# Optimization experiments

Hardware: AMD Instinct MI355X
Metric: run time of the kernel (lower is better)

## Reference

```python
import jax, jax.numpy as jnp
import numpy as np

N_NODES = 100000
E_RAW = 1600000
SKIP_COEFF = 0.5
NEG_SLOPE = 0.2
BN_EPS = 1e-5


def _gat_conv(x, src, dst, W, a_src, a_dst, b, heads, out_ch):
    # PyG GATConv (concat=True). x: [N, F_in], W: [F_in, heads*out_ch]
    N = x.shape[0]
    h = (x @ W).reshape(N, heads, out_ch)                      # [N,H,C]
    alpha_src = jnp.sum(h * a_src, axis=-1)                    # [N,H]
    alpha_dst = jnp.sum(h * a_dst, axis=-1)                    # [N,H]
    e = jax.nn.leaky_relu(alpha_src[src] + alpha_dst[dst], NEG_SLOPE)  # [E,H]
    # segment softmax over incoming edges of each destination node
    m = jax.ops.segment_max(e, dst, num_segments=N)            # [N,H]
    p = jnp.exp(e - m[dst])
    denom = jax.ops.segment_sum(p, dst, num_segments=N)        # [N,H]
    alpha = p / denom[dst]                                      # [E,H]
    out = jax.ops.segment_sum(h[src] * alpha[:, :, None], dst, num_segments=N)
    return out.reshape(N, heads * out_ch) + b


def _bn(x, gamma, beta):
    # BatchNorm1d, training-mode batch statistics (biased variance)
    mu = jnp.mean(x, axis=0)
    var = jnp.var(x, axis=0)
    return (x - mu) * jax.lax.rsqrt(var + BN_EPS) * gamma + beta


def _glorot(key, shape):
    fan = shape[0] + shape[-1] if len(shape) == 2 else shape[-1] * 2
    s = jnp.sqrt(6.0 / fan)
    return jax.random.uniform(key, shape, jnp.float32, -s, s)


def setup_inputs() -> dict:
    key = jax.random.key(0)
    ks = jax.random.split(key, 24)
    x = jax.random.normal(ks[0], (N_NODES, 128), jnp.float32)
    edge_index = jax.random.randint(ks[1], (2, E_RAW), 0, N_NODES, jnp.int64)
    d = {"x": x, "edge_index": edge_index}
    # conv0: 128 -> (4 heads x 32); conv1,conv2: 128 -> (4x32); conv3: 128 -> (1x64)
    dims = [(128, 4, 32), (128, 4, 32), (128, 4, 32), (128, 1, 64)]
    ki = 2
    for l, (fin, H, C) in enumerate(dims):
        d[f"W{l}"] = _glorot(ks[ki], (fin, H * C)); ki += 1
        d[f"as{l}"] = _glorot(ks[ki], (H, C)); ki += 1
        d[f"ad{l}"] = _glorot(ks[ki], (H, C)); ki += 1
        d[f"b{l}"] = jnp.zeros((H * C,), jnp.float32)
    d["g1"] = jnp.ones((128,), jnp.float32)
    d["be1"] = jnp.zeros((128,), jnp.float32)
    d["g2"] = jnp.ones((128,), jnp.float32)
    d["be2"] = jnp.zeros((128,), jnp.float32)
    return d


def reference(x, edge_index, W0, as0, ad0, b0, W1, as1, ad1, b1,
              W2, as2, ad2, b2, W3, as3, ad3, b3, g1, be1, g2, be2):
    N = x.shape[0]
    loops = jnp.arange(N, dtype=edge_index.dtype)
    src = jnp.concatenate([edge_index[0], loops])  # add self-loops (PyG default)
    dst = jnp.concatenate([edge_index[1], loops])

    h = _gat_conv(x, src, dst, W0, as0, ad0, b0, 4, 32)        # [N,128]
    h_skip = h
    # i = 1
    h = _gat_conv(h, src, dst, W1, as1, ad1, b1, 4, 32)
    h = jax.nn.relu(_bn(h, g1, be1))
    out1 = h
    # i = 2 (skip branch)
    h = _gat_conv(h, src, dst, W2, as2, ad2, b2, 4, 32)
    h = _bn(h, g2, be2) + SKIP_COEFF * h_skip
    h = jax.nn.relu(h)
    out2 = h

    h = out1 + out2
    return _gat_conv(h, src, dst, W3, as3, ad3, b3, 1, 64)      # [N,64]
```

## Files before the change

### kernel.cpp

```cpp
#include <hip/hip_runtime.h>
#include <cstdint>
#include <cstddef>


typedef unsigned int uint;
typedef unsigned short ushort_t;
typedef __attribute__((ext_vector_type(8))) short bf16x8_t;
typedef __attribute__((ext_vector_type(4))) float f32x4_t;

__device__ __forceinline__ float leaky(float e) { return e < 0.f ? 0.2f * e : e; }
__device__ __forceinline__ float bflo(uint u) { return __uint_as_float(u << 16); }
__device__ __forceinline__ float bfhi(uint u) { return __uint_as_float(u & 0xffff0000u); }
__device__ __forceinline__ ushort_t f2bf(float f) {
  uint u = __float_as_uint(f);
  u += 0x7fffu + ((u >> 16) & 1u);
  return (ushort_t)(u >> 16);
}
__device__ __forceinline__ float bf2f(ushort_t h) { return __uint_as_float((uint)h << 16); }
__device__ __forceinline__ uint pack2(float a, float b) {
  return (uint)f2bf(a) | ((uint)f2bf(b) << 16);
}


__global__ __launch_bounds__(256) void k_deg(const int* __restrict__ ei, int ER, int ET,
                                             int* __restrict__ deg) {
  int e = blockIdx.x * 256 + threadIdx.x;
  if (e >= ET) return;
  int d = (e < ER) ? ei[ER + e] : (e - ER);
  atomicAdd(&deg[d], 1);
}

__global__ __launch_bounds__(256) void k_scan1(const int* __restrict__ deg, int* __restrict__ rp,
                                               int* __restrict__ bsums, int n) {
  __shared__ int sh[256];
  int tid = threadIdx.x;
  int base = blockIdx.x * 2048 + tid * 8;
  int pre[8];
  int s = 0;
#pragma unroll
  for (int j = 0; j < 8; ++j) {
    int idx = base + j;
    int v = (idx < n) ? deg[idx] : 0;
    pre[j] = s;
    s += v;
  }
  sh[tid] = s;
  __syncthreads();
  for (int d = 1; d < 256; d <<= 1) {
    int t = (tid >= d) ? sh[tid - d] : 0;
    __syncthreads();
    if (tid >= d) sh[tid] += t;
    __syncthreads();
  }
  int excl = sh[tid] - s;
#pragma unroll
  for (int j = 0; j < 8; ++j) {
    int idx = base + j;
    if (idx < n) rp[idx] = excl + pre[j];
  }
  if (tid == 255) bsums[blockIdx.x] = sh[255];
}

__global__ void k_scan2(int* bsums, int nb) {
  for (int i = 1; i < nb; ++i) bsums[i] += bsums[i - 1];
}

__global__ __launch_bounds__(256) void k_scan3(int* __restrict__ rp, const int* __restrict__ bsums,
                                               int n, int ET) {
  int i = blockIdx.x * 256 + threadIdx.x;
  if (i > n) return;
  if (i == n) { rp[n] = ET; return; }
  int b = i >> 11;
  if (b > 0) rp[i] += bsums[b - 1];
}

__global__ __launch_bounds__(256) void k_scatter(const int* __restrict__ ei, int ER, int ET,
                                                 const int* __restrict__ rp, int* __restrict__ fill,
                                                 int* __restrict__ col) {
  int e = blockIdx.x * 256 + threadIdx.x;
  if (e >= ET) return;
  int s, d;
  if (e < ER) { s = ei[e]; d = ei[ER + e]; } else { s = e - ER; d = s; }
  int pos = rp[d] + atomicAdd(&fill[d], 1);
  col[pos] = s;
}


__global__ __launch_bounds__(256) void k_prepW(const float* __restrict__ W0,
                                               const float* __restrict__ W1,
                                               const float* __restrict__ W2,
                                               const float* __restrict__ W3,
                                               ushort_t* __restrict__ Wthi,
                                               ushort_t* __restrict__ Wtlo) {
  int id = blockIdx.x * 256 + threadIdx.x;
  int l = id >> 14;
  if (l >= 4) return;
  int t = id & 16383;
  int j = t >> 7, k = t & 127;
  const float* W = (l == 0) ? W0 : (l == 1) ? W1 : (l == 2) ? W2 : W3;
  int cols = (l == 3) ? 64 : 128;
  if (j >= cols) return;
  float v = W[(size_t)k * cols + j];
  ushort_t hi = f2bf(v);
  float rem = v - bf2f(hi);
  Wthi[(size_t)l * 16384 + j * 128 + k] = hi;
  Wtlo[(size_t)l * 16384 + j * 128 + k] = f2bf(rem);
}


__global__ __launch_bounds__(256) void k_split(const float* __restrict__ in,
                                               uint* __restrict__ hi2, uint* __restrict__ lo2,
                                               int n4) {
  int i = blockIdx.x * 256 + threadIdx.x;
  if (i >= n4) return;
  float4 v = ((const float4*)in)[i];
  ushort_t hx = f2bf(v.x), hy = f2bf(v.y), hz = f2bf(v.z), hw = f2bf(v.w);
  uint2 h = make_uint2((uint)hx | ((uint)hy << 16), (uint)hz | ((uint)hw << 16));
  uint2 l = make_uint2(pack2(v.x - bf2f(hx), v.y - bf2f(hy)),
                       pack2(v.z - bf2f(hz), v.w - bf2f(hw)));
  ((uint2*)hi2)[i] = h;
  ((uint2*)lo2)[i] = l;
}


template <int COLS, int H>
__global__ __launch_bounds__(256) void k_mm(const ushort_t* __restrict__ Ahi,
                                            const ushort_t* __restrict__ Alo,
                                            const ushort_t* __restrict__ Wthi,
                                            const ushort_t* __restrict__ Wtlo,
                                            const float* __restrict__ aS,
                                            const float* __restrict__ aD,
                                            ushort_t* __restrict__ hbf,
                                            float* __restrict__ asg,
                                            float* __restrict__ adg, int N) {
  constexpr int NB = COLS / 16;
  __shared__ __align__(16) ushort_t sWhi[COLS * 136];
  __shared__ __align__(16) ushort_t sWlo[COLS * 136];
  int tid = threadIdx.x;
  int lane = tid & 63, wv = tid >> 6;
  int lj = lane & 15, lg = lane >> 4;
  int r0 = blockIdx.x * 64 + wv * 16;

  for (int idx = tid; idx < COLS * 16; idx += 256) {
    int j = idx >> 4, seg = idx & 15;
    uint4 vh = *(const uint4*)(Wthi + (size_t)j * 128 + seg * 8);
    uint4 vl = *(const uint4*)(Wtlo + (size_t)j * 128 + seg * 8);
    *(uint4*)&sWhi[j * 136 + seg * 8] = vh;
    *(uint4*)&sWlo[j * 136 + seg * 8] = vl;
  }
  __syncthreads();

  f32x4_t acc[NB];
#pragma unroll
  for (int cb = 0; cb < NB; ++cb) acc[cb] = (f32x4_t){0.f, 0.f, 0.f, 0.f};

  int rowc = r0 + lj; if (rowc >= N) rowc = N - 1;
  const ushort_t* apH = Ahi + (size_t)rowc * 128 + lg * 8;
  const ushort_t* apL = Alo + (size_t)rowc * 128 + lg * 8;

#pragma unroll
  for (int kc = 0; kc < 4; ++kc) {
    bf16x8_t ah = *(const bf16x8_t*)(apH + kc * 32);
    bf16x8_t al = *(const bf16x8_t*)(apL + kc * 32);
#pragma unroll
    for (int cb = 0; cb < NB; ++cb) {
      int boff = (cb * 16 + lj) * 136 + kc * 32 + lg * 8;
      bf16x8_t bh = *(const bf16x8_t*)&sWhi[boff];
      bf16x8_t bl = *(const bf16x8_t*)&sWlo[boff];
      acc[cb] = __builtin_amdgcn_mfma_f32_16x16x32_bf16(ah, bh, acc[cb], 0, 0, 0);
      acc[cb] = __builtin_amdgcn_mfma_f32_16x16x32_bf16(al, bh, acc[cb], 0, 0, 0);
      acc[cb] = __builtin_amdgcn_mfma_f32_16x16x32_bf16(ah, bl, acc[cb], 0, 0, 0);
    }
  }

  float asv[NB], adv[NB];
#pragma unroll
  for (int cb = 0; cb < NB; ++cb) {
    asv[cb] = aS[cb * 16 + lj];
    adv[cb] = aD[cb * 16 + lj];
  }
#pragma unroll
  for (int reg = 0; reg < 4; ++reg) {
    int row = r0 + lg * 4 + reg;
    if (H == 4) {
      float ps[4] = {0.f, 0.f, 0.f, 0.f}, pd[4] = {0.f, 0.f, 0.f, 0.f};
#pragma unroll
      for (int cb = 0; cb < NB; ++cb) {
        int h = cb >> 1;
        ps[h] += acc[cb][reg] * asv[cb];
        pd[h] += acc[cb][reg] * adv[cb];
      }
#pragma unroll
      for (int m = 1; m < 16; m <<= 1) {
#pragma unroll
        for (int h = 0; h < 4; ++h) {
          ps[h] += __shfl_xor(ps[h], m);
          pd[h] += __shfl_xor(pd[h], m);
        }
      }
      if (lj == 0 && row < N) {
        *(float4*)(asg + (size_t)row * 4) = make_float4(ps[0], ps[1], ps[2], ps[3]);
        *(float4*)(adg + (size_t)row * 4) = make_float4(pd[0], pd[1], pd[2], pd[3]);
      }
    } else {
      float ps = 0.f, pd = 0.f;
#pragma unroll
      for (int cb = 0; cb < NB; ++cb) {
        ps += acc[cb][reg] * asv[cb];
        pd += acc[cb][reg] * adv[cb];
      }
#pragma unroll
      for (int m = 1; m < 16; m <<= 1) {
        ps += __shfl_xor(ps, m);
        pd += __shfl_xor(pd, m);
      }
      if (lj == 0 && row < N) { asg[row] = ps; adg[row] = pd; }
    }
  }

  __syncthreads();
  ushort_t* bnc = sWhi + wv * (16 * 136);
#pragma unroll
  for (int cb = 0; cb < NB; ++cb)
#pragma unroll
    for (int reg = 0; reg < 4; ++reg)
      bnc[(lg * 4 + reg) * 136 + cb * 16 + lj] = f2bf(acc[cb][reg]);
  constexpr int UPR = COLS / 8;
  constexpr int NPASS = 16 * UPR / 64;
#pragma unroll
  for (int p = 0; p < NPASS; ++p) {
    int u = p * 64 + lane;
    int rl = u / UPR, sg = u % UPR;
    if (r0 + rl < N)
      *(uint4*)(hbf + (size_t)(r0 + rl) * COLS + sg * 8) = *(const uint4*)&bnc[rl * 136 + sg * 8];
  }
}


template <int H, int C, int MODE>
__global__ __launch_bounds__(256) void k_agg(const int* __restrict__ rp, const int* __restrict__ col,
                                             const ushort_t* __restrict__ hbf,
                                             const float* __restrict__ asg,
                                             const float* __restrict__ adg,
                                             const float* __restrict__ bias,
                                             float* __restrict__ out,
                                             uint* __restrict__ outp,
                                             uint* __restrict__ ohi, uint* __restrict__ olo,
                                             int N) {
  constexpr int HC = H * C;
  constexpr int LPE = HC / 8;
  constexpr int EPI = 64 / LPE;
  __shared__ float shp[4][64 * H];
  int lane = threadIdx.x & 63;
  int wv = threadIdx.x >> 6;
  int n = blockIdx.x * 4 + wv;
  if (n >= N) return;

  int sub = lane / LPE;
  int le = lane % LPE;
  int ch0 = le * 8;
  int head = (H == 4) ? (ch0 >> 5) : 0;

  float d0 = 0.f, d1 = 0.f, d2 = 0.f, d3 = 0.f;
  if (H == 4) {
    float4 t = *(const float4*)(adg + (size_t)n * 4);
    d0 = t.x; d1 = t.y; d2 = t.z; d3 = t.w;
  } else {
    d0 = adg[n];
  }

  int s0 = rp[n], s1 = rp[n + 1];
  float denom = 0.f;
  float a[8];
#pragma unroll
  for (int k = 0; k < 8; ++k) a[k] = 0.f;

  for (int base = s0; base < s1; base += 64) {
    int lim = s1 - base; if (lim > 64) lim = 64;
    int j = base + lane;
    bool valid = j < s1;
    int cj = valid ? col[j] : 0;

    if (H == 4) {
      float4 t = *(const float4*)(asg + (size_t)cj * 4);
      float4 p;
      p.x = valid ? __expf(leaky(t.x + d0)) : 0.f;
      p.y = valid ? __expf(leaky(t.y + d1)) : 0.f;
      p.z = valid ? __expf(leaky(t.z + d2)) : 0.f;
      p.w = valid ? __expf(leaky(t.w + d3)) : 0.f;
      *(float4*)&shp[wv][lane * 4] = p;
    } else {
      float t = asg[cj];
      shp[wv][lane] = valid ? __expf(leaky(t + d0)) : 0.f;
    }
    __builtin_amdgcn_sched_barrier(0);

    for (int i = 0; i < lim; i += EPI) {
      int e = i + sub;
      int s = __shfl(cj, e);
      float p = (H == 4) ? shp[wv][e * 4 + head] : shp[wv][e];
      uint4 hv = *(const uint4*)(hbf + (size_t)s * HC + ch0);
      a[0] += p * bflo(hv.x); a[1] += p * bfhi(hv.x);
      a[2] += p * bflo(hv.y); a[3] += p * bfhi(hv.y);
      a[4] += p * bflo(hv.z); a[5] += p * bfhi(hv.z);
      a[6] += p * bflo(hv.w); a[7] += p * bfhi(hv.w);
      denom += p;
    }
  }

#pragma unroll
  for (int m = LPE; m < 64; m <<= 1) {
#pragma unroll
    for (int k = 0; k < 8; ++k) a[k] += __shfl_xor(a[k], m);
    denom += __shfl_xor(denom, m);
  }

  if (sub != 0) return;
  float inv = 1.f / denom;
  float o[8];
#pragma unroll
  for (int k = 0; k < 8; ++k) o[k] = a[k] * inv + bias[ch0 + k];

  if (MODE == 0) {
    float4 w0 = make_float4(o[0], o[1], o[2], o[3]);
    float4 w1 = make_float4(o[4], o[5], o[6], o[7]);
    *(float4*)(out + (size_t)n * HC + ch0) = w0;
    *(float4*)(out + (size_t)n * HC + ch0 + 4) = w1;
  } else {
    uint hw[4], lw[4];
#pragma unroll
    for (int k = 0; k < 4; ++k) {
      ushort_t hx = f2bf(o[2 * k]), hy = f2bf(o[2 * k + 1]);
      hw[k] = (uint)hx | ((uint)hy << 16);
      lw[k] = pack2(o[2 * k] - bf2f(hx), o[2 * k + 1] - bf2f(hy));
    }
    uint4 hv = make_uint4(hw[0], hw[1], hw[2], hw[3]);
    uint4 lv = make_uint4(lw[0], lw[1], lw[2], lw[3]);
    *(uint4*)(outp + (size_t)n * 64 + le * 4) = hv;
    *(uint4*)(ohi + (size_t)n * 64 + le * 4) = hv;
    *(uint4*)(olo + (size_t)n * 64 + le * 4) = lv;
  }
}


__global__ __launch_bounds__(512) void k_bnstats1(const float* __restrict__ t,
                                                  float* __restrict__ p1, float* __restrict__ p2,
                                                  int N) {
  __shared__ float ls[4][128], ls2[4][128];
  int c = threadIdx.x & 127, q = threadIdx.x >> 7;
  float s = 0.f, s2 = 0.f;
  for (int r = blockIdx.x * 4 + q; r < N; r += gridDim.x * 4) {
    float v = t[(size_t)r * 128 + c];
    s += v;
    s2 += v * v;
  }
  ls[q][c] = s; ls2[q][c] = s2;
  __syncthreads();
  if (q == 0) {
    s = ls[0][c] + ls[1][c] + ls[2][c] + ls[3][c];
    s2 = ls2[0][c] + ls2[1][c] + ls2[2][c] + ls2[3][c];
    p1[blockIdx.x * 128 + c] = s;
    p2[blockIdx.x * 128 + c] = s2;
  }
}

__global__ void k_bnstats2(const float* __restrict__ p1, const float* __restrict__ p2,
                           float* __restrict__ mu, float* __restrict__ rstd, int G, int N) {
  int c = threadIdx.x;
  float s = 0.f, s2 = 0.f;
  for (int b = 0; b < G; ++b) { s += p1[b * 128 + c]; s2 += p2[b * 128 + c]; }
  float m = s / (float)N;
  float var = s2 / (float)N - m * m;
  mu[c] = m;
  rstd[c] = rsqrtf(var + 1e-5f);
}

__global__ __launch_bounds__(256) void k_bnapply1(const float* __restrict__ t,
                                                  const float* __restrict__ mu,
                                                  const float* __restrict__ rstd,
                                                  const float* __restrict__ g,
                                                  const float* __restrict__ be,
                                                  uint* __restrict__ o1p,
                                                  uint* __restrict__ ohi, uint* __restrict__ olo,
                                                  int n4) {
  int i = blockIdx.x * 256 + threadIdx.x;
  if (i >= n4) return;
  float4 v = ((const float4*)t)[i];
  int c = (i & 31) * 4;
  float4 r;
  r.x = fmaxf((v.x - mu[c + 0]) * rstd[c + 0] * g[c + 0] + be[c + 0], 0.f);
  r.y = fmaxf((v.y - mu[c + 1]) * rstd[c + 1] * g[c + 1] + be[c + 1], 0.f);
  r.z = fmaxf((v.z - mu[c + 2]) * rstd[c + 2] * g[c + 2] + be[c + 2], 0.f);
  r.w = fmaxf((v.w - mu[c + 3]) * rstd[c + 3] * g[c + 3] + be[c + 3], 0.f);
  ushort_t hx = f2bf(r.x), hy = f2bf(r.y), hz = f2bf(r.z), hw = f2bf(r.w);
  uint2 h = make_uint2((uint)hx | ((uint)hy << 16), (uint)hz | ((uint)hw << 16));
  ((uint2*)o1p)[i] = h;
  ((uint2*)ohi)[i] = h;
  ((uint2*)olo)[i] = make_uint2(pack2(r.x - bf2f(hx), r.y - bf2f(hy)),
                                pack2(r.z - bf2f(hz), r.w - bf2f(hw)));
}

__global__ __launch_bounds__(256) void k_bnapply2(const float* __restrict__ t,
                                                  const uint* __restrict__ skp,
                                                  const uint* __restrict__ o1p,
                                                  const float* __restrict__ mu,
                                                  const float* __restrict__ rstd,
                                                  const float* __restrict__ g,
                                                  const float* __restrict__ be,
                                                  uint* __restrict__ ohi, uint* __restrict__ olo,
                                                  int n4) {
  int i = blockIdx.x * 256 + threadIdx.x;
  if (i >= n4) return;
  float4 v = ((const float4*)t)[i];
  uint2 sku = ((const uint2*)skp)[i];
  uint2 o1u = ((const uint2*)o1p)[i];
  int c = (i & 31) * 4;
  float4 r;
  r.x = bflo(o1u.x) + fmaxf((v.x - mu[c + 0]) * rstd[c + 0] * g[c + 0] + be[c + 0] + 0.5f * bflo(sku.x), 0.f);
  r.y = bfhi(o1u.x) + fmaxf((v.y - mu[c + 1]) * rstd[c + 1] * g[c + 1] + be[c + 1] + 0.5f * bfhi(sku.x), 0.f);
  r.z = bflo(o1u.y) + fmaxf((v.z - mu[c + 2]) * rstd[c + 2] * g[c + 2] + be[c + 2] + 0.5f * bflo(sku.y), 0.f);
  r.w = bfhi(o1u.y) + fmaxf((v.w - mu[c + 3]) * rstd[c + 3] * g[c + 3] + be[c + 3] + 0.5f * bfhi(sku.y), 0.f);
  ushort_t hx = f2bf(r.x), hy = f2bf(r.y), hz = f2bf(r.z), hw = f2bf(r.w);
  ((uint2*)ohi)[i] = make_uint2((uint)hx | ((uint)hy << 16), (uint)hz | ((uint)hw << 16));
  ((uint2*)olo)[i] = make_uint2(pack2(r.x - bf2f(hx), r.y - bf2f(hy)),
                                pack2(r.z - bf2f(hz), r.w - bf2f(hw)));
}


extern "C" void kernel_launch(void* const* d_in, const int* in_sizes, int n_in,
                              void* d_out, int out_size, void* d_ws, size_t ws_size,
                              hipStream_t stream) {
  const float* x = (const float*)d_in[0];
  const int* ei = (const int*)d_in[1];
  const float* W[4]  = {(const float*)d_in[2], (const float*)d_in[6],
                        (const float*)d_in[10], (const float*)d_in[14]};
  const float* AS[4] = {(const float*)d_in[3], (const float*)d_in[7],
                        (const float*)d_in[11], (const float*)d_in[15]};
  const float* AD[4] = {(const float*)d_in[4], (const float*)d_in[8],
                        (const float*)d_in[12], (const float*)d_in[16]};
  const float* B[4]  = {(const float*)d_in[5], (const float*)d_in[9],
                        (const float*)d_in[13], (const float*)d_in[17]};
  const float* g1 = (const float*)d_in[18];
  const float* be1 = (const float*)d_in[19];
  const float* g2 = (const float*)d_in[20];
  const float* be2 = (const float*)d_in[21];

  const int N = in_sizes[0] / 128;
  const int ER = in_sizes[1] / 2;
  const int ET = ER + N;

  char* ws = (char*)d_ws;
  size_t off = 0;
  auto carve = [&](size_t bytes) {
    size_t o = off;
    off = (off + bytes + 255) & ~(size_t)255;
    return (void*)(ws + o);
  };
  int* rowptr     = (int*)carve((size_t)(N + 1) * 4);
  int* col        = (int*)carve((size_t)ET * 4);
  int* bsums      = (int*)carve(64 * 4);
  float* asg      = (float*)carve((size_t)N * 4 * 4);
  float* adg      = (float*)carve((size_t)N * 4 * 4);
  ushort_t* hbf   = (ushort_t*)carve((size_t)N * 128 * 2);
  ushort_t* ahi   = (ushort_t*)carve((size_t)N * 128 * 2);
  ushort_t* alo   = (ushort_t*)carve((size_t)N * 128 * 2);
  uint* skipb     = (uint*)carve((size_t)N * 64 * 4);
  uint* out1b     = (uint*)carve((size_t)N * 64 * 4);
  float* tbuf     = (float*)carve((size_t)N * 128 * 4);
  ushort_t* Wthi  = (ushort_t*)carve(4 * 16384 * 2);
  ushort_t* Wtlo  = (ushort_t*)carve(4 * 16384 * 2);
  float* p1       = (float*)carve(128 * 128 * 4);
  float* p2       = (float*)carve(128 * 128 * 4);
  float* mu       = (float*)carve(128 * 4);
  float* rstd     = (float*)carve(128 * 4);
  int* fill       = (int*)asg;
  (void)ws_size;

  const int nb = (N + 2047) / 2048;
  const int gE = (ET + 255) / 256;
  const int gN4 = (N + 3) / 4;
  const int gM = (N + 63) / 64;
  const int n4 = N * 32;
  const int gP = (n4 + 255) / 256;

  hipMemsetAsync(fill, 0, (size_t)N * 4, stream);
  k_deg<<<gE, 256, 0, stream>>>(ei, ER, ET, fill);
  k_scan1<<<nb, 256, 0, stream>>>(fill, rowptr, bsums, N);
  k_scan2<<<1, 1, 0, stream>>>(bsums, nb);
  k_scan3<<<(N + 256) / 256, 256, 0, stream>>>(rowptr, bsums, N, ET);
  hipMemsetAsync(fill, 0, (size_t)N * 4, stream);
  k_scatter<<<gE, 256, 0, stream>>>(ei, ER, ET, rowptr, fill, col);
  k_prepW<<<256, 256, 0, stream>>>(W[0], W[1], W[2], W[3], Wthi, Wtlo);
  k_split<<<gP, 256, 0, stream>>>(x, (uint*)ahi, (uint*)alo, n4);

  k_mm<128, 4><<<gM, 256, 0, stream>>>(ahi, alo, Wthi, Wtlo, AS[0], AD[0], hbf, asg, adg, N);
  k_agg<4, 32, 1><<<gN4, 256, 0, stream>>>(rowptr, col, hbf, asg, adg, B[0], nullptr,
                                           skipb, (uint*)ahi, (uint*)alo, N);

  k_mm<128, 4><<<gM, 256, 0, stream>>>(ahi, alo, Wthi + 16384, Wtlo + 16384, AS[1], AD[1],
                                       hbf, asg, adg, N);
  k_agg<4, 32, 0><<<gN4, 256, 0, stream>>>(rowptr, col, hbf, asg, adg, B[1], tbuf,
                                           nullptr, nullptr, nullptr, N);
  k_bnstats1<<<128, 512, 0, stream>>>(tbuf, p1, p2, N);
  k_bnstats2<<<1, 128, 0, stream>>>(p1, p2, mu, rstd, 128, N);
  k_bnapply1<<<gP, 256, 0, stream>>>(tbuf, mu, rstd, g1, be1, out1b, (uint*)ahi, (uint*)alo, n4);

  k_mm<128, 4><<<gM, 256, 0, stream>>>(ahi, alo, Wthi + 2 * 16384, Wtlo + 2 * 16384, AS[2], AD[2],
                                       hbf, asg, adg, N);
  k_agg<4, 32, 0><<<gN4, 256, 0, stream>>>(rowptr, col, hbf, asg, adg, B[2], tbuf,
                                           nullptr, nullptr, nullptr, N);
  k_bnstats1<<<128, 512, 0, stream>>>(tbuf, p1, p2, N);
  k_bnstats2<<<1, 128, 0, stream>>>(p1, p2, mu, rstd, 128, N);
  k_bnapply2<<<gP, 256, 0, stream>>>(tbuf, skipb, out1b, mu, rstd, g2, be2,
                                     (uint*)ahi, (uint*)alo, n4);

  k_mm<64, 1><<<gM, 256, 0, stream>>>(ahi, alo, Wthi + 3 * 16384, Wtlo + 3 * 16384, AS[3], AD[3],
                                      hbf, asg, adg, N);
  k_agg<1, 64, 0><<<gN4, 256, 0, stream>>>(rowptr, col, hbf, asg, adg, B[3], (float*)d_out,
                                           nullptr, nullptr, nullptr, N);
}
```

Baseline: 916.2 us.

## Fold attention vectors into weight matrix and fuse input split into GEMM

Precomputes W·a_src and W·a_dst as extra columns appended to each transposed weight matrix, so the attention logits come straight out of the MFMA accumulators. This replaces the per-row dot products and shuffle reductions. The first layer now converts fp32 x to bf16 hi/lo pairs inside the GEMM, which removes the separate split kernel and its round trip through memory. BN statistics use 256 blocks instead of 128, and the changed algebra order slightly alters the rounding of the logits.

```diff
diff --git a/kernel.cpp b/kernel.cpp
--- a/kernel.cpp
+++ b/kernel.cpp
@@ -90,58 +90,63 @@
                                                const float* __restrict__ W1,
                                                const float* __restrict__ W2,
                                                const float* __restrict__ W3,
+                                               const float* __restrict__ AS0,
+                                               const float* __restrict__ AS1,
+                                               const float* __restrict__ AS2,
+                                               const float* __restrict__ AS3,
+                                               const float* __restrict__ AD0,
+                                               const float* __restrict__ AD1,
+                                               const float* __restrict__ AD2,
+                                               const float* __restrict__ AD3,
                                                ushort_t* __restrict__ Wthi,
                                                ushort_t* __restrict__ Wtlo) {
   int id = blockIdx.x * 256 + threadIdx.x;
-  int l = id >> 14;
-  if (l >= 4) return;
-  int t = id & 16383;
+  if (id >= 4 * 144 * 128) return;
+  int l = id / (144 * 128);
+  int t = id % (144 * 128);
   int j = t >> 7, k = t & 127;
-  const float* W = (l == 0) ? W0 : (l == 1) ? W1 : (l == 2) ? W2 : W3;
+  const float* W  = (l == 0) ? W0  : (l == 1) ? W1  : (l == 2) ? W2  : W3;
+  const float* aS = (l == 0) ? AS0 : (l == 1) ? AS1 : (l == 2) ? AS2 : AS3;
+  const float* aD = (l == 0) ? AD0 : (l == 1) ? AD1 : (l == 2) ? AD2 : AD3;
   int cols = (l == 3) ? 64 : 128;
-  if (j >= cols) return;
-  float v = W[(size_t)k * cols + j];
+  int H = (l == 3) ? 1 : 4;
+  int C = (l == 3) ? 64 : 32;
+  float v = 0.f;
+  if (j < cols) {
+    v = W[(size_t)k * cols + j];
+  } else if (j < cols + H) {
+    int h = j - cols;
+    for (int c = 0; c < C; ++c) v += W[(size_t)k * cols + h * C + c] * aS[h * C + c];
+  } else if (j < cols + 2 * H) {
+    int h = j - cols - H;
+    for (int c = 0; c < C; ++c) v += W[(size_t)k * cols + h * C + c] * aD[h * C + c];
+  }
   ushort_t hi = f2bf(v);
   float rem = v - bf2f(hi);
-  Wthi[(size_t)l * 16384 + j * 128 + k] = hi;
-  Wtlo[(size_t)l * 16384 + j * 128 + k] = f2bf(rem);
-}
-
-
-__global__ __launch_bounds__(256) void k_split(const float* __restrict__ in,
-                                               uint* __restrict__ hi2, uint* __restrict__ lo2,
-                                               int n4) {
-  int i = blockIdx.x * 256 + threadIdx.x;
-  if (i >= n4) return;
-  float4 v = ((const float4*)in)[i];
-  ushort_t hx = f2bf(v.x), hy = f2bf(v.y), hz = f2bf(v.z), hw = f2bf(v.w);
-  uint2 h = make_uint2((uint)hx | ((uint)hy << 16), (uint)hz | ((uint)hw << 16));
-  uint2 l = make_uint2(pack2(v.x - bf2f(hx), v.y - bf2f(hy)),
-                       pack2(v.z - bf2f(hz), v.w - bf2f(hw)));
-  ((uint2*)hi2)[i] = h;
-  ((uint2*)lo2)[i] = l;
-}
-
-
-template <int COLS, int H>
-__global__ __launch_bounds__(256) void k_mm(const ushort_t* __restrict__ Ahi,
+  Wthi[(size_t)l * 144 * 128 + j * 128 + k] = hi;
+  Wtlo[(size_t)l * 144 * 128 + j * 128 + k] = f2bf(rem);
+}
+
+
+template <int COLS, int CP, int H, int SRC>
+__global__ __launch_bounds__(256) void k_mm(const float* __restrict__ Xf,
+                                            const ushort_t* __restrict__ Ahi,
                                             const ushort_t* __restrict__ Alo,
                                             const ushort_t* __restrict__ Wthi,
                                             const ushort_t* __restrict__ Wtlo,
-                                            const float* __restrict__ aS,
-                                            const float* __restrict__ aD,
                                             ushort_t* __restrict__ hbf,
                                             float* __restrict__ asg,
                                             float* __restrict__ adg, int N) {
-  constexpr int NB = COLS / 16;
-  __shared__ __align__(16) ushort_t sWhi[COLS * 136];
-  __shared__ __align__(16) ushort_t sWlo[COLS * 136];
+  constexpr int NB = CP / 16;
+  constexpr int NBH = COLS / 16;
+  __shared__ __align__(16) ushort_t sWhi[CP * 136];
+  __shared__ __align__(16) ushort_t sWlo[CP * 136];
   int tid = threadIdx.x;
   int lane = tid & 63, wv = tid >> 6;
   int lj = lane & 15, lg = lane >> 4;
   int r0 = blockIdx.x * 64 + wv * 16;
 
-  for (int idx = tid; idx < COLS * 16; idx += 256) {
+  for (int idx = tid; idx < CP * 16; idx += 256) {
     int j = idx >> 4, seg = idx & 15;
     uint4 vh = *(const uint4*)(Wthi + (size_t)j * 128 + seg * 8);
     uint4 vl = *(const uint4*)(Wtlo + (size_t)j * 128 + seg * 8);
@@ -155,13 +160,25 @@
   for (int cb = 0; cb < NB; ++cb) acc[cb] = (f32x4_t){0.f, 0.f, 0.f, 0.f};
 
   int rowc = r0 + lj; if (rowc >= N) rowc = N - 1;
-  const ushort_t* apH = Ahi + (size_t)rowc * 128 + lg * 8;
-  const ushort_t* apL = Alo + (size_t)rowc * 128 + lg * 8;
 
 #pragma unroll
   for (int kc = 0; kc < 4; ++kc) {
-    bf16x8_t ah = *(const bf16x8_t*)(apH + kc * 32);
-    bf16x8_t al = *(const bf16x8_t*)(apL + kc * 32);
+    bf16x8_t ah, al;
+    if (SRC == 1) {
+      const float* xp = Xf + (size_t)rowc * 128 + kc * 32 + lg * 8;
+      float xv[8];
+      *(float4*)&xv[0] = *(const float4*)xp;
+      *(float4*)&xv[4] = *(const float4*)(xp + 4);
+#pragma unroll
+      for (int e = 0; e < 8; ++e) {
+        ushort_t hi = f2bf(xv[e]);
+        ah[e] = (short)hi;
+        al[e] = (short)f2bf(xv[e] - bf2f(hi));
+      }
+    } else {
+      ah = *(const bf16x8_t*)(Ahi + (size_t)rowc * 128 + kc * 32 + lg * 8);
+      al = *(const bf16x8_t*)(Alo + (size_t)rowc * 128 + kc * 32 + lg * 8);
+    }
 #pragma unroll
     for (int cb = 0; cb < NB; ++cb) {
       int boff = (cb * 16 + lj) * 136 + kc * 32 + lg * 8;
@@ -173,55 +190,25 @@
     }
   }
 
-  float asv[NB], adv[NB];
-#pragma unroll
-  for (int cb = 0; cb < NB; ++cb) {
-    asv[cb] = aS[cb * 16 + lj];
-    adv[cb] = aD[cb * 16 + lj];
-  }
 #pragma unroll
   for (int reg = 0; reg < 4; ++reg) {
     int row = r0 + lg * 4 + reg;
-    if (H == 4) {
-      float ps[4] = {0.f, 0.f, 0.f, 0.f}, pd[4] = {0.f, 0.f, 0.f, 0.f};
-#pragma unroll
-      for (int cb = 0; cb < NB; ++cb) {
-        int h = cb >> 1;
-        ps[h] += acc[cb][reg] * asv[cb];
-        pd[h] += acc[cb][reg] * adv[cb];
+    if (row < N) {
+      float av = acc[NBH][reg];
+      if (H == 4) {
+        if (lj < 4) asg[(size_t)row * 4 + lj] = av;
+        else if (lj < 8) adg[(size_t)row * 4 + (lj - 4)] = av;
+      } else {
+        if (lj == 0) asg[row] = av;
+        else if (lj == 1) adg[row] = av;
       }
-#pragma unroll
-      for (int m = 1; m < 16; m <<= 1) {
-#pragma unroll
-        for (int h = 0; h < 4; ++h) {
-          ps[h] += __shfl_xor(ps[h], m);
-          pd[h] += __shfl_xor(pd[h], m);
-        }
-      }
-      if (lj == 0 && row < N) {
-        *(float4*)(asg + (size_t)row * 4) = make_float4(ps[0], ps[1], ps[2], ps[3]);
-        *(float4*)(adg + (size_t)row * 4) = make_float4(pd[0], pd[1], pd[2], pd[3]);
-      }
-    } else {
-      float ps = 0.f, pd = 0.f;
-#pragma unroll
-      for (int cb = 0; cb < NB; ++cb) {
-        ps += acc[cb][reg] * asv[cb];
-        pd += acc[cb][reg] * adv[cb];
-      }
-#pragma unroll
-      for (int m = 1; m < 16; m <<= 1) {
-        ps += __shfl_xor(ps, m);
-        pd += __shfl_xor(pd, m);
-      }
-      if (lj == 0 && row < N) { asg[row] = ps; adg[row] = pd; }
     }
   }
 
   __syncthreads();
   ushort_t* bnc = sWhi + wv * (16 * 136);
 #pragma unroll
-  for (int cb = 0; cb < NB; ++cb)
+  for (int cb = 0; cb < NBH; ++cb)
 #pragma unroll
     for (int reg = 0; reg < 4; ++reg)
       bnc[(lg * 4 + reg) * 136 + cb * 16 + lj] = f2bf(acc[cb][reg]);
@@ -467,10 +454,10 @@
   uint* skipb     = (uint*)carve((size_t)N * 64 * 4);
   uint* out1b     = (uint*)carve((size_t)N * 64 * 4);
   float* tbuf     = (float*)carve((size_t)N * 128 * 4);
-  ushort_t* Wthi  = (ushort_t*)carve(4 * 16384 * 2);
-  ushort_t* Wtlo  = (ushort_t*)carve(4 * 16384 * 2);
-  float* p1       = (float*)carve(128 * 128 * 4);
-  float* p2       = (float*)carve(128 * 128 * 4);
+  ushort_t* Wthi  = (ushort_t*)carve(4 * 144 * 128 * 2);
+  ushort_t* Wtlo  = (ushort_t*)carve(4 * 144 * 128 * 2);
+  float* p1       = (float*)carve(256 * 128 * 4);
+  float* p2       = (float*)carve(256 * 128 * 4);
   float* mu       = (float*)carve(128 * 4);
   float* rstd     = (float*)carve(128 * 4);
   int* fill       = (int*)asg;
@@ -482,6 +469,7 @@
   const int gM = (N + 63) / 64;
   const int n4 = N * 32;
   const int gP = (n4 + 255) / 256;
+  const int gW = (4 * 144 * 128 + 255) / 256;
 
   hipMemsetAsync(fill, 0, (size_t)N * 4, stream);
   k_deg<<<gE, 256, 0, stream>>>(ei, ER, ET, fill);
@@ -490,32 +478,37 @@
   k_scan3<<<(N + 256) / 256, 256, 0, stream>>>(rowptr, bsums, N, ET);
   hipMemsetAsync(fill, 0, (size_t)N * 4, stream);
   k_scatter<<<gE, 256, 0, stream>>>(ei, ER, ET, rowptr, fill, col);
-  k_prepW<<<256, 256, 0, stream>>>(W[0], W[1], W[2], W[3], Wthi, Wtlo);
-  k_split<<<gP, 256, 0, stream>>>(x, (uint*)ahi, (uint*)alo, n4);
-
-  k_mm<128, 4><<<gM, 256, 0, stream>>>(ahi, alo, Wthi, Wtlo, AS[0], AD[0], hbf, asg, adg, N);
+  k_prepW<<<gW, 256, 0, stream>>>(W[0], W[1], W[2], W[3],
+                                  AS[0], AS[1], AS[2], AS[3],
+                                  AD[0], AD[1], AD[2], AD[3], Wthi, Wtlo);
+
+  k_mm<128, 144, 4, 1><<<gM, 256, 0, stream>>>(x, nullptr, nullptr,
+                                               Wthi, Wtlo, hbf, asg, adg, N);
   k_agg<4, 32, 1><<<gN4, 256, 0, stream>>>(rowptr, col, hbf, asg, adg, B[0], nullptr,
                                            skipb, (uint*)ahi, (uint*)alo, N);
 
-  k_mm<128, 4><<<gM, 256, 0, stream>>>(ahi, alo, Wthi + 16384, Wtlo + 16384, AS[1], AD[1],
-                                       hbf, asg, adg, N);
+  k_mm<128, 144, 4, 0><<<gM, 256, 0, stream>>>(nullptr, ahi, alo,
+                                               Wthi + 144 * 128, Wtlo + 144 * 128,
+                                               hbf, asg, adg, N);
   k_agg<4, 32, 0><<<gN4, 256, 0, stream>>>(rowptr, col, hbf, asg, adg, B[1], tbuf,
                                            nullptr, nullptr, nullptr, N);
-  k_bnstats1<<<128, 512, 0, stream>>>(tbuf, p1, p2, N);
-  k_bnstats2<<<1, 128, 0, stream>>>(p1, p2, mu, rstd, 128, N);
+  k_bnstats1<<<256, 512, 0, stream>>>(tbuf, p1, p2, N);
+  k_bnstats2<<<1, 128, 0, stream>>>(p1, p2, mu, rstd, 256, N);
   k_bnapply1<<<gP, 256, 0, stream>>>(tbuf, mu, rstd, g1, be1, out1b, (uint*)ahi, (uint*)alo, n4);
 
-  k_mm<128, 4><<<gM, 256, 0, stream>>>(ahi, alo, Wthi + 2 * 16384, Wtlo + 2 * 16384, AS[2], AD[2],
-                                       hbf, asg, adg, N);
+  k_mm<128, 144, 4, 0><<<gM, 256, 0, stream>>>(nullptr, ahi, alo,
+                                               Wthi + 2 * 144 * 128, Wtlo + 2 * 144 * 128,
+                                               hbf, asg, adg, N);
   k_agg<4, 32, 0><<<gN4, 256, 0, stream>>>(rowptr, col, hbf, asg, adg, B[2], tbuf,
                                            nullptr, nullptr, nullptr, N);
-  k_bnstats1<<<128, 512, 0, stream>>>(tbuf, p1, p2, N);
-  k_bnstats2<<<1, 128, 0, stream>>>(p1, p2, mu, rstd, 128, N);
+  k_bnstats1<<<256, 512, 0, stream>>>(tbuf, p1, p2, N);
+  k_bnstats2<<<1, 128, 0, stream>>>(p1, p2, mu, rstd, 256, N);
   k_bnapply2<<<gP, 256, 0, stream>>>(tbuf, skipb, out1b, mu, rstd, g2, be2,
                                      (uint*)ahi, (uint*)alo, n4);
 
-  k_mm<64, 1><<<gM, 256, 0, stream>>>(ahi, alo, Wthi + 3 * 16384, Wtlo + 3 * 16384, AS[3], AD[3],
-                                      hbf, asg, adg, N);
+  k_mm<64, 80, 1, 0><<<gM, 256, 0, stream>>>(nullptr, ahi, alo,
+                                             Wthi + 3 * 144 * 128, Wtlo + 3 * 144 * 128,
+                                             hbf, asg, adg, N);
   k_agg<1, 64, 0><<<gN4, 256, 0, stream>>>(rowptr, col, hbf, asg, adg, B[3], (float*)d_out,
                                            nullptr, nullptr, nullptr, N);
 }
```

After: 915.7 us. Within noise of the previous version (-0.1%).
